# Performance work log

Hardware: AMD Instinct MI355X
Metric: run time of the kernel (lower is better)

Reference implementation:

```python
import jax, jax.numpy as jnp
import numpy as np

VOCAB, E, H, P, B, S = 30522, 1024, 1024, 16, 32, 256
HD = H // 2  # per-direction LSTM hidden


def _lstm_dir(xt, Wih, Whh, bih, bhh, reverse):
    # xt: [S,B,in]; PyTorch gate order i,f,g,o
    Hd = Whh.shape[1]
    Bz = xt.shape[1]
    bias = bih + bhh

    def step(carry, xb):
        h, c = carry
        g = xb @ Wih.T + h @ Whh.T + bias
        i, f, gg, o = jnp.split(g, 4, axis=-1)
        c = jax.nn.sigmoid(f) * c + jax.nn.sigmoid(i) * jnp.tanh(gg)
        h = jax.nn.sigmoid(o) * jnp.tanh(c)
        return (h, c), h

    init = (jnp.zeros((Bz, Hd), xt.dtype), jnp.zeros((Bz, Hd), xt.dtype))
    _, hs = jax.lax.scan(step, init, xt, reverse=reverse)
    return hs  # [S,B,Hd], time-ordered


def _bilstm(x, Wih, Whh, bih, bhh):
    # x: [B,S,in]; Wih: [2,4*HD,in] (dir 0 = fwd, dir 1 = bwd)
    xt = jnp.swapaxes(x, 0, 1)
    fw = _lstm_dir(xt, Wih[0], Whh[0], bih[0], bhh[0], False)
    bw = _lstm_dir(xt, Wih[1], Whh[1], bih[1], bhh[1], True)
    return jnp.swapaxes(jnp.concatenate([fw, bw], axis=-1), 0, 1)  # [B,S,2*HD]


def setup_inputs() -> dict:
    key = jax.random.key(0)
    ks = jax.random.split(key, 20)
    sc = 0.05
    inp = {}
    inp["emb"] = jax.random.normal(ks[0], (VOCAB, E), jnp.float32) * sc
    inp["ctx_emb"] = jax.random.normal(ks[1], (VOCAB, E), jnp.float32) * sc
    inp["prompt_emb"] = jax.random.normal(ks[2], (P, E), jnp.float32) * sc
    # LSTM layer 0: input E; layer 1: input 2*HD = H
    inp["Wih0"] = jax.random.normal(ks[3], (2, 4 * HD, E), jnp.float32) * sc
    inp["Whh0"] = jax.random.normal(ks[4], (2, 4 * HD, HD), jnp.float32) * sc
    inp["bih0"] = jax.random.normal(ks[5], (2, 4 * HD), jnp.float32) * sc
    inp["bhh0"] = jax.random.normal(ks[6], (2, 4 * HD), jnp.float32) * sc
    inp["Wih1"] = jax.random.normal(ks[7], (2, 4 * HD, H), jnp.float32) * sc
    inp["Whh1"] = jax.random.normal(ks[8], (2, 4 * HD, HD), jnp.float32) * sc
    inp["bih1"] = jax.random.normal(ks[9], (2, 4 * HD), jnp.float32) * sc
    inp["bhh1"] = jax.random.normal(ks[10], (2, 4 * HD), jnp.float32) * sc
    inp["W1"] = jax.random.normal(ks[11], (H, H), jnp.float32) * sc
    inp["b1"] = jnp.zeros((H,), jnp.float32)
    inp["W2"] = jax.random.normal(ks[12], (E, H), jnp.float32) * sc
    inp["b2"] = jnp.zeros((E,), jnp.float32)
    inp["input_ids"] = jax.random.randint(ks[13], (B, S), 0, VOCAB)
    # distinct, sorted prompt positions per batch row (torch loop assumes valid slots)
    pk = jax.random.split(ks[14], B)
    perms = jax.vmap(lambda k: jax.random.permutation(k, S)[:P])(pk)
    inp["prompt_indexes"] = jnp.sort(perms, axis=1)
    return inp


def reference(emb, ctx_emb, prompt_emb, Wih0, Whh0, bih0, bhh0,
              Wih1, Whh1, bih1, bhh1, W1, b1, W2, b2,
              input_ids, prompt_indexes):
    raw = emb[input_ids]                               # [B,S,E]
    b_idx = jnp.arange(input_ids.shape[0])[:, None]    # [B,1]
    # unique_prompt branch: detached raw + ctx embedding, scatter prompt embeds
    allb = jax.lax.stop_gradient(raw) + ctx_emb[input_ids]
    allb = allb.at[b_idx, prompt_indexes].set(
        jnp.broadcast_to(prompt_emb, (input_ids.shape[0],) + prompt_emb.shape))
    h = _bilstm(allb, Wih0, Whh0, bih0, bhh0)
    h = _bilstm(h, Wih1, Whh1, bih1, bhh1)             # [B,S,H]
    out = jax.nn.relu(h @ W1.T + b1) @ W2.T + b2       # [B,S,E]
    upd = out[b_idx, prompt_indexes] + prompt_emb      # [B,P,E]
    return raw.at[b_idx, prompt_indexes].set(upd)
```

## Files before the change

### kernel.cpp

```cpp
#include <hip/hip_runtime.h>
#include <hip/hip_bf16.h>
#include <math.h>

constexpr int NB  = 32;
constexpr int NS  = 256;
constexpr int NE  = 1024;
constexpr int NH  = 1024;
constexpr int NHD = 512;
constexpr int NG  = 2048;
constexpr int NP  = 16;
constexpr int NBS = NB * NS;
constexpr int GK  = 1024;

constexpr int UPW  = 16;
constexpr int NWGD = NHD / UPW;
constexpr size_t GT_DIR = (size_t)NWGD * 256 * 2048;

typedef __attribute__((ext_vector_type(8))) short bf16x8;
typedef __attribute__((ext_vector_type(4))) float f32x4;
typedef unsigned short u16;

__device__ __forceinline__ float sigm(float x) { return 1.0f / (1.0f + __expf(-x)); }
__device__ __forceinline__ u16 f2bf(float f) {
    union { float f; unsigned u; } v; v.f = f;
    unsigned r = v.u + 0x7FFF + ((v.u >> 16) & 1);
    return (u16)(r >> 16);
}
__device__ __forceinline__ float bf2f(u16 b) {
    return __uint_as_float((unsigned)b << 16);
}

__global__ void k_zero(int* p) { p[blockIdx.x * 256 + threadIdx.x] = 0; }

__global__ void k_allb(const float* __restrict__ emb, const float* __restrict__ ctx,
                       const float* __restrict__ pemb, const int* __restrict__ ids,
                       const int* __restrict__ pidx, u16* __restrict__ allb) {
    int r = blockIdx.x;
    int b = r >> 8, s = r & 255;
    __shared__ int ppos;
    if (threadIdx.x == 0) {
        int t = -1;
        #pragma unroll
        for (int p = 0; p < NP; ++p)
            if (pidx[b * NP + p] == s) t = p;
        ppos = t;
    }
    __syncthreads();
    int e = threadIdx.x;
    float4 v;
    if (ppos >= 0) {
        v = ((const float4*)(pemb + (size_t)ppos * NE))[e];
    } else {
        int id = ids[r];
        float4 a = ((const float4*)(emb + (size_t)id * NE))[e];
        float4 c = ((const float4*)(ctx + (size_t)id * NE))[e];
        v = make_float4(a.x + c.x, a.y + c.y, a.z + c.z, a.w + c.w);
    }
    ushort4 o;
    o.x = f2bf(v.x); o.y = f2bf(v.y); o.z = f2bf(v.z); o.w = f2bf(v.w);
    *(ushort4*)(allb + ((size_t)(s * NB + b)) * NE + e * 4) = o;
}

__global__ void k_raw(const float* __restrict__ emb, const int* __restrict__ ids,
                      float* __restrict__ out) {
    int r = blockIdx.x;
    int id = ids[r];
    ((float4*)(out + (size_t)r * NE))[threadIdx.x] =
        ((const float4*)(emb + (size_t)id * NE))[threadIdx.x];
}

__global__ void k_wcvt(const float* __restrict__ Wih, const float* __restrict__ bih,
                       const float* __restrict__ bhh, u16* __restrict__ Wbf,
                       float* __restrict__ biasC) {
    int blk = blockIdx.x;
    int d = blk >> 11, np = blk & 2047;
    int rw = (np & 3) * 512 + (np >> 2);
    const float* src = Wih + ((size_t)d * NG + rw) * GK;
    u16* dst = Wbf + ((size_t)d * NG + np) * GK;
    int t = threadIdx.x;
    float4 v = ((const float4*)src)[t];
    ushort4 o;
    o.x = f2bf(v.x); o.y = f2bf(v.y); o.z = f2bf(v.z); o.w = f2bf(v.w);
    ((ushort4*)dst)[t] = o;
    if (t == 0)
        biasC[d * NG + np] = bih[d * NG + rw] + bhh[d * NG + rw];
}

__global__ __launch_bounds__(256) void k_gemm_m(const u16* __restrict__ A0,
                                                const u16* __restrict__ A1,
                                                int astride,
                                                const u16* __restrict__ W,
                                                const float* __restrict__ bc,
                                                float* __restrict__ Gt) {
    __shared__ char At[128 * 128];
    __shared__ char Wt[128 * 128];
    int tid = threadIdx.x;
    int lane = tid & 63, w = tid >> 6;
    int n0 = blockIdx.x * 128, m0 = blockIdx.y * 128;
    int r = tid >> 1, h = tid & 1;

    f32x4 acc[4][4];
    #pragma unroll
    for (int i = 0; i < 4; ++i)
        #pragma unroll
        for (int j = 0; j < 4; ++j) acc[i][j] = (f32x4){0.f, 0.f, 0.f, 0.f};

    unsigned rsw = (unsigned)((r & 7) << 4);
    for (int kt = 0; kt < GK; kt += 64) {
        {
            int k0 = kt + h * 32;
            const u16* asrc = (k0 < 512) ? (A0 + (size_t)(m0 + r) * astride + k0)
                                         : (A1 + (size_t)(m0 + r) * astride + (k0 - 512));
            const u16* wsrc = W + (size_t)(n0 + r) * GK + k0;
            #pragma unroll
            for (int j = 0; j < 4; ++j) {
                uint4 va = *(const uint4*)(asrc + j * 8);
                *(uint4*)(At + r * 128 + (((unsigned)(h * 64 + j * 16)) ^ rsw)) = va;
                uint4 vw = *(const uint4*)(wsrc + j * 8);
                *(uint4*)(Wt + r * 128 + (((unsigned)(h * 64 + j * 16)) ^ rsw)) = vw;
            }
        }
        __syncthreads();
        #pragma unroll
        for (int sub = 0; sub < 2; ++sub) {
            bf16x8 af[4], bfr[4];
            int kbyte = sub * 64 + (lane >> 4) * 16;
            #pragma unroll
            for (int ni = 0; ni < 4; ++ni) {
                int rr = (w & 1) * 64 + ni * 16 + (lane & 15);
                af[ni] = *(const bf16x8*)(Wt + rr * 128 + ((unsigned)kbyte ^ ((unsigned)((rr & 7) << 4))));
            }
            #pragma unroll
            for (int mi = 0; mi < 4; ++mi) {
                int rr = (w >> 1) * 64 + mi * 16 + (lane & 15);
                bfr[mi] = *(const bf16x8*)(At + rr * 128 + ((unsigned)kbyte ^ ((unsigned)((rr & 7) << 4))));
            }
            #pragma unroll
            for (int mi = 0; mi < 4; ++mi)
                #pragma unroll
                for (int ni = 0; ni < 4; ++ni)
                    acc[mi][ni] = __builtin_amdgcn_mfma_f32_16x16x32_bf16(
                        af[ni], bfr[mi], acc[mi][ni], 0, 0, 0);
        }
        __syncthreads();
    }
    #pragma unroll
    for (int mi = 0; mi < 4; ++mi) {
        int mp = m0 + (w >> 1) * 64 + mi * 16 + (lane & 15);
        int t = mp >> 5, b = mp & 31;
        #pragma unroll
        for (int ni = 0; ni < 4; ++ni) {
            int npb = n0 + (w & 1) * 64 + ni * 16 + (lane >> 4) * 4;
            int unit = npb >> 2;
            float4 bv = *(const float4*)(bc + npb);
            f32x4 a = acc[mi][ni];
            float4 o = make_float4(a[0] + bv.x, a[1] + bv.y, a[2] + bv.z, a[3] + bv.w);
            *(float4*)(Gt + ((size_t)((unit >> 4) * NS + t)) * 2048 + b * 64 + (unit & 15) * 4) = o;
        }
    }
}

__global__ __launch_bounds__(256) void k_lstm_p(const float* __restrict__ Gt,
                                                const float* __restrict__ Whh,
                                                u16* __restrict__ hxb,
                                                int* __restrict__ cblk) {
    __shared__ char hlds[NB * NHD * 2];
    int wg = blockIdx.x;
    int d = wg & 1;
    int slice = wg >> 1;
    int n0 = slice * UPW;
    int tid = threadIdx.x;
    int lane = tid & 63;
    int w = tid >> 6;
    int* lines  = cblk + d * 512;
    int* myline = lines + slice * 16;
    int pollidx = (lane & 31) * 16;
    u16* hxd = hxb + (size_t)d * NS * NB * NHD;
    const float* Gd = Gt + (size_t)d * GT_DIR + (size_t)slice * NS * 2048;

    bf16x8 wfrag[16];
    {
        int rloc = lane & 15;
        int usub = rloc >> 2, g = rloc & 3;
        int kb = lane >> 4;
        const float* wrow = Whh + ((size_t)d * NG + g * NHD + n0 + 4 * w + usub) * NHD;
        #pragma unroll
        for (int kk = 0; kk < 16; ++kk) {
            const float* p = wrow + kk * 32 + kb * 8;
            float4 x = *(const float4*)p;
            float4 y = *(const float4*)(p + 4);
            bf16x8 wf;
            wf[0] = (short)f2bf(x.x); wf[1] = (short)f2bf(x.y);
            wf[2] = (short)f2bf(x.z); wf[3] = (short)f2bf(x.w);
            wf[4] = (short)f2bf(y.x); wf[5] = (short)f2bf(y.y);
            wf[6] = (short)f2bf(y.z); wf[7] = (short)f2bf(y.w);
            wfrag[kk] = wf;
        }
    }
    int uloc  = 4 * w + (lane >> 4);
    int unitC = n0 + uloc;
    int bcol0 = lane & 15;
    int bcol1 = 16 + bcol0;
    int kb    = lane >> 4;
    int c8 = tid & 7, bRow = tid >> 3;

    float c0 = 0.f, c1 = 0.f;
    int ttp = d ? (NS - 1) : 0;
    float4 Gv0 = *(const float4*)(Gd + (size_t)ttp * 2048 + bcol0 * 64 + uloc * 4);
    float4 Gv1 = *(const float4*)(Gd + (size_t)ttp * 2048 + bcol1 * 64 + uloc * 4);

    for (int step = 0; step < NS; ++step) {
        int tt = d ? (NS - 1 - step) : step;
        f32x4 acc0 = {0.f, 0.f, 0.f, 0.f};
        f32x4 acc1 = {0.f, 0.f, 0.f, 0.f};
        if (step) {
            int tprev = d ? tt + 1 : tt - 1;
            const u16* srow = hxd + ((size_t)tprev * NB + bRow) * NHD;
            char* dstrow = hlds + bRow * 1024;
            unsigned rsw = (unsigned)((bRow & 7) << 4);
            #pragma unroll
            for (int i = 0; i < 8; ++i) {
                uint4 v = *(const uint4*)(srow + c8 * 64 + i * 8);
                *(uint4*)(dstrow + (((unsigned)(c8 * 128 + i * 16)) ^ rsw)) = v;
            }
            __syncthreads();
            const char* b0base = hlds + bcol0 * 1024;
            const char* b1base = hlds + bcol1 * 1024;
            unsigned s0 = (unsigned)((bcol0 & 7) << 4);
            unsigned s1 = (unsigned)((bcol1 & 7) << 4);
            #pragma unroll
            for (int kk = 0; kk < 16; ++kk) {
                bf16x8 b0 = *(const bf16x8*)(b0base + (((unsigned)(kk * 64 + kb * 16)) ^ s0));
                bf16x8 b1 = *(const bf16x8*)(b1base + (((unsigned)(kk * 64 + kb * 16)) ^ s1));
                acc0 = __builtin_amdgcn_mfma_f32_16x16x32_bf16(wfrag[kk], b0, acc0, 0, 0, 0);
                acc1 = __builtin_amdgcn_mfma_f32_16x16x32_bf16(wfrag[kk], b1, acc1, 0, 0, 0);
            }
        }
        {
            float ig = sigm(acc0[0] + Gv0.x);
            float fg = sigm(acc0[1] + Gv0.y);
            float gg = tanhf(acc0[2] + Gv0.z);
            float og = sigm(acc0[3] + Gv0.w);
            c0 = fg * c0 + ig * gg;
            float hv = og * tanhf(c0);
            __hip_atomic_store(hxd + ((size_t)tt * NB + bcol0) * NHD + unitC, f2bf(hv),
                               __ATOMIC_RELAXED, __HIP_MEMORY_SCOPE_AGENT);
        }
        {
            float ig = sigm(acc1[0] + Gv1.x);
            float fg = sigm(acc1[1] + Gv1.y);
            float gg = tanhf(acc1[2] + Gv1.z);
            float og = sigm(acc1[3] + Gv1.w);
            c1 = fg * c1 + ig * gg;
            float hv = og * tanhf(c1);
            __hip_atomic_store(hxd + ((size_t)tt * NB + bcol1) * NHD + unitC, f2bf(hv),
                               __ATOMIC_RELAXED, __HIP_MEMORY_SCOPE_AGENT);
        }
        if (step == NS - 1) break;
        asm volatile("s_waitcnt vmcnt(0)" ::: "memory");
        __syncthreads();
        if (tid == 0)
            __hip_atomic_store(myline, step + 1, __ATOMIC_RELAXED,
                               __HIP_MEMORY_SCOPE_AGENT);
        {
            int ttn = d ? tt - 1 : tt + 1;
            Gv0 = *(const float4*)(Gd + (size_t)ttn * 2048 + bcol0 * 64 + uloc * 4);
            Gv1 = *(const float4*)(Gd + (size_t)ttn * 2048 + bcol1 * 64 + uloc * 4);
        }
        asm volatile("" ::: "memory");
        {
            int target = step + 1;
            for (;;) {
                int v = __hip_atomic_load(lines + pollidx, __ATOMIC_RELAXED,
                                          __HIP_MEMORY_SCOPE_AGENT);
                if (__all(v >= target)) break;
                __builtin_amdgcn_s_sleep(1);
            }
        }
    }
}

__global__ __launch_bounds__(256) void k_mlp1(const u16* __restrict__ hxb,
                                              const int* __restrict__ pidx,
                                              const float* __restrict__ W1,
                                              const float* __restrict__ b1,
                                              float* __restrict__ mid) {
    __shared__ float As[16][65];
    __shared__ float Ws[16][65];
    int tid = threadIdx.x;
    int tx = tid & 15, ty = tid >> 4;
    int n0 = blockIdx.x * 64, m0 = blockIdx.y * 64;
    int lr = tid >> 2;
    int lk = (tid & 3) * 4;
    int m = m0 + lr;
    int bb = m >> 4;
    int s = pidx[m];
    float acc[4][4] = {};
    for (int kt = 0; kt < GK; kt += 16) {
        int k0 = kt + lk;
        int half = k0 >> 9;
        ushort4 av4 = *(const ushort4*)(hxb + (((size_t)(half * NS + s)) * NB + bb) * NHD + (k0 & 511));
        float4 wv = *(const float4*)(W1 + (size_t)(n0 + lr) * GK + k0);
        As[lk + 0][lr] = bf2f(av4.x); As[lk + 1][lr] = bf2f(av4.y);
        As[lk + 2][lr] = bf2f(av4.z); As[lk + 3][lr] = bf2f(av4.w);
        Ws[lk + 0][lr] = wv.x; Ws[lk + 1][lr] = wv.y;
        Ws[lk + 2][lr] = wv.z; Ws[lk + 3][lr] = wv.w;
        __syncthreads();
        #pragma unroll
        for (int kk = 0; kk < 16; ++kk) {
            float a[4], wv2[4];
            #pragma unroll
            for (int i = 0; i < 4; ++i) a[i] = As[kk][ty * 4 + i];
            #pragma unroll
            for (int j = 0; j < 4; ++j) wv2[j] = Ws[kk][tx * 4 + j];
            #pragma unroll
            for (int i = 0; i < 4; ++i)
                #pragma unroll
                for (int j = 0; j < 4; ++j) acc[i][j] += a[i] * wv2[j];
        }
        __syncthreads();
    }
    #pragma unroll
    for (int j = 0; j < 4; ++j) {
        int n = n0 + tx * 4 + j;
        float bias = b1[n];
        #pragma unroll
        for (int i = 0; i < 4; ++i)
            mid[(size_t)(m0 + ty * 4 + i) * 1024 + n] = fmaxf(acc[i][j] + bias, 0.f);
    }
}

__global__ __launch_bounds__(256) void k_mlp2(const float* __restrict__ mid,
                                              const int* __restrict__ pidx,
                                              const float* __restrict__ W2,
                                              const float* __restrict__ b2,
                                              const float* __restrict__ pemb,
                                              float* __restrict__ out) {
    __shared__ float As[16][65];
    __shared__ float Ws[16][65];
    int tid = threadIdx.x;
    int tx = tid & 15, ty = tid >> 4;
    int n0 = blockIdx.x * 64, m0 = blockIdx.y * 64;
    int lr = tid >> 2;
    int lk = (tid & 3) * 4;
    float acc[4][4] = {};
    for (int kt = 0; kt < GK; kt += 16) {
        float4 av = *(const float4*)(mid + (size_t)(m0 + lr) * GK + kt + lk);
        float4 wv = *(const float4*)(W2 + (size_t)(n0 + lr) * GK + kt + lk);
        As[lk + 0][lr] = av.x; As[lk + 1][lr] = av.y;
        As[lk + 2][lr] = av.z; As[lk + 3][lr] = av.w;
        Ws[lk + 0][lr] = wv.x; Ws[lk + 1][lr] = wv.y;
        Ws[lk + 2][lr] = wv.z; Ws[lk + 3][lr] = wv.w;
        __syncthreads();
        #pragma unroll
        for (int kk = 0; kk < 16; ++kk) {
            float a[4], wv2[4];
            #pragma unroll
            for (int i = 0; i < 4; ++i) a[i] = As[kk][ty * 4 + i];
            #pragma unroll
            for (int j = 0; j < 4; ++j) wv2[j] = Ws[kk][tx * 4 + j];
            #pragma unroll
            for (int i = 0; i < 4; ++i)
                #pragma unroll
                for (int j = 0; j < 4; ++j) acc[i][j] += a[i] * wv2[j];
        }
        __syncthreads();
    }
    #pragma unroll
    for (int i = 0; i < 4; ++i) {
        int m = m0 + ty * 4 + i;
        int bb = m >> 4, p = m & 15;
        int s = pidx[m];
        float* orow = out + ((size_t)(bb * NS + s)) * NE;
        const float* prow = pemb + (size_t)p * NE;
        #pragma unroll
        for (int j = 0; j < 4; ++j) {
            int n = n0 + tx * 4 + j;
            orow[n] = acc[i][j] + b2[n] + prow[n];
        }
    }
}

extern "C" void kernel_launch(void* const* d_in, const int* in_sizes, int n_in,
                              void* d_out, int out_size, void* d_ws, size_t ws_size,
                              hipStream_t stream) {
    const float* emb  = (const float*)d_in[0];
    const float* ctx  = (const float*)d_in[1];
    const float* pemb = (const float*)d_in[2];
    const float* Wih0 = (const float*)d_in[3];
    const float* Whh0 = (const float*)d_in[4];
    const float* bih0 = (const float*)d_in[5];
    const float* bhh0 = (const float*)d_in[6];
    const float* Wih1 = (const float*)d_in[7];
    const float* Whh1 = (const float*)d_in[8];
    const float* bih1 = (const float*)d_in[9];
    const float* bhh1 = (const float*)d_in[10];
    const float* W1   = (const float*)d_in[11];
    const float* b1   = (const float*)d_in[12];
    const float* W2   = (const float*)d_in[13];
    const float* b2   = (const float*)d_in[14];
    const int* ids    = (const int*)d_in[15];
    const int* pidx   = (const int*)d_in[16];
    float* out = (float*)d_out;

    char* ws = (char*)d_ws;
    float* Gt    = (float*)ws;
    u16*   allb  = (u16*)(ws + 134217728u);
    u16*   hx    = (u16*)(ws + 150994944u);
    u16*   Wbf   = (u16*)(ws + 167772160u);
    float* biasC = (float*)(ws + 176160768u);
    float* mid   = (float*)(ws + 176177152u);
    int*   ctr   = (int*)(ws + 178274304u);

    k_zero<<<dim3(8), dim3(256), 0, stream>>>(ctr);
    k_allb<<<dim3(NBS), dim3(256), 0, stream>>>(emb, ctx, pemb, ids, pidx, allb);

    k_wcvt<<<dim3(2 * NG), dim3(256), 0, stream>>>(Wih0, bih0, bhh0, Wbf, biasC);
    for (int d = 0; d < 2; ++d)
        k_gemm_m<<<dim3(NG / 128, NBS / 128), dim3(256), 0, stream>>>(
            allb, allb + 512, 1024, Wbf + (size_t)d * NG * GK, biasC + d * NG,
            Gt + (size_t)d * GT_DIR);
    k_lstm_p<<<dim3(2 * NWGD), dim3(256), 0, stream>>>(Gt, Whh0, hx, ctr);

    k_raw<<<dim3(NBS), dim3(256), 0, stream>>>(emb, ids, out);

    k_wcvt<<<dim3(2 * NG), dim3(256), 0, stream>>>(Wih1, bih1, bhh1, Wbf, biasC);
    for (int d = 0; d < 2; ++d)
        k_gemm_m<<<dim3(NG / 128, NBS / 128), dim3(256), 0, stream>>>(
            hx, hx + (size_t)NS * NB * NHD, 512, Wbf + (size_t)d * NG * GK,
            biasC + d * NG, Gt + (size_t)d * GT_DIR);
    k_lstm_p<<<dim3(2 * NWGD), dim3(256), 0, stream>>>(Gt, Whh1, hx, ctr + 1024);

    k_mlp1<<<dim3(16, 8), dim3(256), 0, stream>>>(hx, pidx, W1, b1, mid);
    k_mlp2<<<dim3(16, 8), dim3(256), 0, stream>>>(mid, pidx, W2, b2, pemb, out);
}
```

Baseline: 2.363 ms.

## Double LSTM units per workgroup to halve recurrent WG count, use fast tanh

The persistent LSTM recurrence kernel now handles 32 hidden units per workgroup with 512 threads, so each direction uses 16 workgroups instead of 32. The gate-buffer layout in the GEMM epilogue changes to match, and each workgroup still stages the full h tile into LDS. This cuts the number of workgroups that must poll the cross-workgroup barrier each timestep, which reduces sync latency. tanh and sigmoid switch to fast exp/fdividef forms, trading some accuracy for cheaper transcendentals in the serial critical path.

```diff
diff --git a/kernel.cpp b/kernel.cpp
--- a/kernel.cpp
+++ b/kernel.cpp
@@ -12,15 +12,22 @@
 constexpr int NBS = NB * NS;
 constexpr int GK  = 1024;
 
-constexpr int UPW  = 16;
+constexpr int UPW  = 32;
 constexpr int NWGD = NHD / UPW;
-constexpr size_t GT_DIR = (size_t)NWGD * 256 * 2048;
+constexpr size_t GT_DIR = (size_t)NWGD * 256 * 4096;
 
 typedef __attribute__((ext_vector_type(8))) short bf16x8;
 typedef __attribute__((ext_vector_type(4))) float f32x4;
 typedef unsigned short u16;
-
-__device__ __forceinline__ float sigm(float x) { return 1.0f / (1.0f + __expf(-x)); }
+typedef unsigned long long u64;
+
+__device__ __forceinline__ float sigm(float x) {
+    return __fdividef(1.0f, 1.0f + __expf(-x));
+}
+__device__ __forceinline__ float tanhfast(float x) {
+    float t = __expf(2.0f * x);
+    return 1.0f - __fdividef(2.0f, t + 1.0f);
+}
 __device__ __forceinline__ u16 f2bf(float f) {
     union { float f; unsigned u; } v; v.f = f;
     unsigned r = v.u + 0x7FFF + ((v.u >> 16) & 1);
@@ -155,12 +162,12 @@
             float4 bv = *(const float4*)(bc + npb);
             f32x4 a = acc[mi][ni];
             float4 o = make_float4(a[0] + bv.x, a[1] + bv.y, a[2] + bv.z, a[3] + bv.w);
-            *(float4*)(Gt + ((size_t)((unit >> 4) * NS + t)) * 2048 + b * 64 + (unit & 15) * 4) = o;
-        }
-    }
-}
-
-__global__ __launch_bounds__(256) void k_lstm_p(const float* __restrict__ Gt,
+            *(float4*)(Gt + ((size_t)((unit >> 5) * NS + t)) * 4096 + b * 128 + (unit & 31) * 4) = o;
+        }
+    }
+}
+
+__global__ __launch_bounds__(512) void k_lstm_v(const float* __restrict__ Gt,
                                                 const float* __restrict__ Whh,
                                                 u16* __restrict__ hxb,
                                                 int* __restrict__ cblk) {
@@ -172,21 +179,21 @@
     int tid = threadIdx.x;
     int lane = tid & 63;
     int w = tid >> 6;
-    int* lines  = cblk + d * 512;
+    int* lines  = cblk + d * 256;
     int* myline = lines + slice * 16;
-    int pollidx = (lane & 31) * 16;
+    int pollidx = (lane & 15) * 16;
     u16* hxd = hxb + (size_t)d * NS * NB * NHD;
-    const float* Gd = Gt + (size_t)d * GT_DIR + (size_t)slice * NS * 2048;
+    const float* Gd = Gt + (size_t)d * GT_DIR + (size_t)slice * NS * 4096;
 
     bf16x8 wfrag[16];
     {
         int rloc = lane & 15;
         int usub = rloc >> 2, g = rloc & 3;
-        int kb = lane >> 4;
+        int kb0 = lane >> 4;
         const float* wrow = Whh + ((size_t)d * NG + g * NHD + n0 + 4 * w + usub) * NHD;
         #pragma unroll
         for (int kk = 0; kk < 16; ++kk) {
-            const float* p = wrow + kk * 32 + kb * 8;
+            const float* p = wrow + kk * 32 + kb0 * 8;
             float4 x = *(const float4*)p;
             float4 y = *(const float4*)(p + 4);
             bf16x8 wf;
@@ -202,12 +209,15 @@
     int bcol0 = lane & 15;
     int bcol1 = 16 + bcol0;
     int kb    = lane >> 4;
-    int c8 = tid & 7, bRow = tid >> 3;
+    int sRow = tid >> 4, c4 = tid & 15;
+    unsigned rsw = (unsigned)((sRow & 7) << 4);
+    unsigned s0 = (unsigned)((bcol0 & 7) << 4);
+    unsigned s1 = (unsigned)((bcol1 & 7) << 4);
 
     float c0 = 0.f, c1 = 0.f;
     int ttp = d ? (NS - 1) : 0;
-    float4 Gv0 = *(const float4*)(Gd + (size_t)ttp * 2048 + bcol0 * 64 + uloc * 4);
-    float4 Gv1 = *(const float4*)(Gd + (size_t)ttp * 2048 + bcol1 * 64 + uloc * 4);
+    float4 Gv0 = *(const float4*)(Gd + (size_t)ttp * 4096 + bcol0 * 128 + uloc * 4);
+    float4 Gv1 = *(const float4*)(Gd + (size_t)ttp * 4096 + bcol1 * 128 + uloc * 4);
 
     for (int step = 0; step < NS; ++step) {
         int tt = d ? (NS - 1 - step) : step;
@@ -215,19 +225,16 @@
         f32x4 acc1 = {0.f, 0.f, 0.f, 0.f};
         if (step) {
             int tprev = d ? tt + 1 : tt - 1;
-            const u16* srow = hxd + ((size_t)tprev * NB + bRow) * NHD;
-            char* dstrow = hlds + bRow * 1024;
-            unsigned rsw = (unsigned)((bRow & 7) << 4);
-            #pragma unroll
-            for (int i = 0; i < 8; ++i) {
-                uint4 v = *(const uint4*)(srow + c8 * 64 + i * 8);
-                *(uint4*)(dstrow + (((unsigned)(c8 * 128 + i * 16)) ^ rsw)) = v;
+            const u16* srow = hxd + ((size_t)tprev * NB + sRow) * NHD + c4 * 32;
+            char* dstrow = hlds + sRow * 1024;
+            #pragma unroll
+            for (int i = 0; i < 4; ++i) {
+                uint4 v = *(const uint4*)(srow + i * 8);
+                *(uint4*)(dstrow + (((unsigned)(c4 * 64 + i * 16)) ^ rsw)) = v;
             }
             __syncthreads();
             const char* b0base = hlds + bcol0 * 1024;
             const char* b1base = hlds + bcol1 * 1024;
-            unsigned s0 = (unsigned)((bcol0 & 7) << 4);
-            unsigned s1 = (unsigned)((bcol1 & 7) << 4);
             #pragma unroll
             for (int kk = 0; kk < 16; ++kk) {
                 bf16x8 b0 = *(const bf16x8*)(b0base + (((unsigned)(kk * 64 + kb * 16)) ^ s0));
@@ -239,20 +246,20 @@
         {
             float ig = sigm(acc0[0] + Gv0.x);
             float fg = sigm(acc0[1] + Gv0.y);
-            float gg = tanhf(acc0[2] + Gv0.z);
+            float gg = tanhfast(acc0[2] + Gv0.z);
             float og = sigm(acc0[3] + Gv0.w);
             c0 = fg * c0 + ig * gg;
-            float hv = og * tanhf(c0);
+            float hv = og * tanhfast(c0);
             __hip_atomic_store(hxd + ((size_t)tt * NB + bcol0) * NHD + unitC, f2bf(hv),
                                __ATOMIC_RELAXED, __HIP_MEMORY_SCOPE_AGENT);
         }
         {
             float ig = sigm(acc1[0] + Gv1.x);
             float fg = sigm(acc1[1] + Gv1.y);
-            float gg = tanhf(acc1[2] + Gv1.z);
+            float gg = tanhfast(acc1[2] + Gv1.z);
             float og = sigm(acc1[3] + Gv1.w);
             c1 = fg * c1 + ig * gg;
-            float hv = og * tanhf(c1);
+            float hv = og * tanhfast(c1);
             __hip_atomic_store(hxd + ((size_t)tt * NB + bcol1) * NHD + unitC, f2bf(hv),
                                __ATOMIC_RELAXED, __HIP_MEMORY_SCOPE_AGENT);
         }
@@ -264,8 +271,8 @@
                                __HIP_MEMORY_SCOPE_AGENT);
         {
             int ttn = d ? tt - 1 : tt + 1;
-            Gv0 = *(const float4*)(Gd + (size_t)ttn * 2048 + bcol0 * 64 + uloc * 4);
-            Gv1 = *(const float4*)(Gd + (size_t)ttn * 2048 + bcol1 * 64 + uloc * 4);
+            Gv0 = *(const float4*)(Gd + (size_t)ttn * 4096 + bcol0 * 128 + uloc * 4);
+            Gv1 = *(const float4*)(Gd + (size_t)ttn * 4096 + bcol1 * 128 + uloc * 4);
         }
         asm volatile("" ::: "memory");
         {
@@ -412,7 +419,7 @@
     float* mid   = (float*)(ws + 176177152u);
     int*   ctr   = (int*)(ws + 178274304u);
 
-    k_zero<<<dim3(8), dim3(256), 0, stream>>>(ctr);
+    k_zero<<<dim3(4), dim3(256), 0, stream>>>(ctr);
     k_allb<<<dim3(NBS), dim3(256), 0, stream>>>(emb, ctx, pemb, ids, pidx, allb);
 
     k_wcvt<<<dim3(2 * NG), dim3(256), 0, stream>>>(Wih0, bih0, bhh0, Wbf, biasC);
@@ -420,7 +427,7 @@
         k_gemm_m<<<dim3(NG / 128, NBS / 128), dim3(256), 0, stream>>>(
             allb, allb + 512, 1024, Wbf + (size_t)d * NG * GK, biasC + d * NG,
             Gt + (size_t)d * GT_DIR);
-    k_lstm_p<<<dim3(2 * NWGD), dim3(256), 0, stream>>>(Gt, Whh0, hx, ctr);
+    k_lstm_v<<<dim3(2 * NWGD), dim3(512), 0, stream>>>(Gt, Whh0, hx, ctr);
 
     k_raw<<<dim3(NBS), dim3(256), 0, stream>>>(emb, ids, out);
 
@@ -429,7 +436,7 @@
         k_gemm_m<<<dim3(NG / 128, NBS / 128), dim3(256), 0, stream>>>(
             hx, hx + (size_t)NS * NB * NHD, 512, Wbf + (size_t)d * NG * GK,
             biasC + d * NG, Gt + (size_t)d * GT_DIR);
-    k_lstm_p<<<dim3(2 * NWGD), dim3(256), 0, stream>>>(Gt, Whh1, hx, ctr + 1024);
+    k_lstm_v<<<dim3(2 * NWGD), dim3(512), 0, stream>>>(Gt, Whh1, hx, ctr + 512);
 
     k_mlp1<<<dim3(16, 8), dim3(256), 0, stream>>>(hx, pidx, W1, b1, mid);
     k_mlp2<<<dim3(16, 8), dim3(256), 0, stream>>>(mid, pidx, W2, b2, pemb, out);
```

New measurement: 2.409 ms. No clear change (+2.0%).

## Fuse input-projection GEMM with LSTM recurrence via per-timestep-group readiness counters

Applied to the files above, without the earlier changes.

Merges the input-gate GEMM and the persistent LSTM recurrence into one launch. GEMM blocks publish completion counters per 128-row (4-timestep) group, ordered so each direction's needed timesteps are produced first, and the recurrence blocks spin on those counters before reading gate preactivations. This lets the serial recurrence start while the GEMM is still running. The raw-embedding copy is folded into the same launch, and the layer-1 output gets its own buffer (reusing allb). Sigmoid and tanh switch to fast exp/divide approximations. The design depends on the 64 recurrence workgroups being resident and scheduled ahead of the GEMM blocks; otherwise it can deadlock or lose the overlap.

```diff
diff --git a/kernel.cpp b/kernel.cpp
--- a/kernel.cpp
+++ b/kernel.cpp
@@ -19,8 +19,15 @@
 typedef __attribute__((ext_vector_type(8))) short bf16x8;
 typedef __attribute__((ext_vector_type(4))) float f32x4;
 typedef unsigned short u16;
-
-__device__ __forceinline__ float sigm(float x) { return 1.0f / (1.0f + __expf(-x)); }
+typedef unsigned long long u64;
+
+__device__ __forceinline__ float sigm(float x) {
+    return __fdividef(1.0f, 1.0f + __expf(-x));
+}
+__device__ __forceinline__ float tanhfast(float x) {
+    float t = __expf(2.0f * x);
+    return 1.0f - __fdividef(2.0f, t + 1.0f);
+}
 __device__ __forceinline__ u16 f2bf(float f) {
     union { float f; unsigned u; } v; v.f = f;
     unsigned r = v.u + 0x7FFF + ((v.u >> 16) & 1);
@@ -59,14 +66,6 @@
     ushort4 o;
     o.x = f2bf(v.x); o.y = f2bf(v.y); o.z = f2bf(v.z); o.w = f2bf(v.w);
     *(ushort4*)(allb + ((size_t)(s * NB + b)) * NE + e * 4) = o;
-}
-
-__global__ void k_raw(const float* __restrict__ emb, const int* __restrict__ ids,
-                      float* __restrict__ out) {
-    int r = blockIdx.x;
-    int id = ids[r];
-    ((float4*)(out + (size_t)r * NE))[threadIdx.x] =
-        ((const float4*)(emb + (size_t)id * NE))[threadIdx.x];
 }
 
 __global__ void k_wcvt(const float* __restrict__ Wih, const float* __restrict__ bih,
@@ -86,94 +85,120 @@
         biasC[d * NG + np] = bih[d * NG + rw] + bhh[d * NG + rw];
 }
 
-__global__ __launch_bounds__(256) void k_gemm_m(const u16* __restrict__ A0,
-                                                const u16* __restrict__ A1,
-                                                int astride,
-                                                const u16* __restrict__ W,
-                                                const float* __restrict__ bc,
-                                                float* __restrict__ Gt) {
-    __shared__ char At[128 * 128];
-    __shared__ char Wt[128 * 128];
+__global__ __launch_bounds__(256) void k_mega(
+        const u16* __restrict__ A0, const u16* __restrict__ A1, int astride,
+        const u16* __restrict__ Wbf, const float* __restrict__ biasC,
+        float* __restrict__ Gt, const float* __restrict__ Whh,
+        u16* __restrict__ hxb, int* __restrict__ ctrL,
+        const float* __restrict__ emb, const int* __restrict__ ids,
+        float* __restrict__ rawout) {
+    __shared__ char smem[32768];
+    int wg = blockIdx.x;
     int tid = threadIdx.x;
-    int lane = tid & 63, w = tid >> 6;
-    int n0 = blockIdx.x * 128, m0 = blockIdx.y * 128;
-    int r = tid >> 1, h = tid & 1;
-
-    f32x4 acc[4][4];
-    #pragma unroll
-    for (int i = 0; i < 4; ++i)
-        #pragma unroll
-        for (int j = 0; j < 4; ++j) acc[i][j] = (f32x4){0.f, 0.f, 0.f, 0.f};
-
-    unsigned rsw = (unsigned)((r & 7) << 4);
-    for (int kt = 0; kt < GK; kt += 64) {
-        {
-            int k0 = kt + h * 32;
-            const u16* asrc = (k0 < 512) ? (A0 + (size_t)(m0 + r) * astride + k0)
-                                         : (A1 + (size_t)(m0 + r) * astride + (k0 - 512));
-            const u16* wsrc = W + (size_t)(n0 + r) * GK + k0;
-            #pragma unroll
-            for (int j = 0; j < 4; ++j) {
-                uint4 va = *(const uint4*)(asrc + j * 8);
-                *(uint4*)(At + r * 128 + (((unsigned)(h * 64 + j * 16)) ^ rsw)) = va;
-                uint4 vw = *(const uint4*)(wsrc + j * 8);
-                *(uint4*)(Wt + r * 128 + (((unsigned)(h * 64 + j * 16)) ^ rsw)) = vw;
-            }
-        }
-        __syncthreads();
-        #pragma unroll
-        for (int sub = 0; sub < 2; ++sub) {
-            bf16x8 af[4], bfr[4];
-            int kbyte = sub * 64 + (lane >> 4) * 16;
+
+    if (wg >= 2112) {
+        int r = wg - 2112;
+        int id = ids[r];
+        ((float4*)(rawout + (size_t)r * NE))[tid] =
+            ((const float4*)(emb + (size_t)id * NE))[tid];
+        return;
+    }
+
+    if (wg >= 64) {
+        char* At = smem;
+        char* Wt = smem + 16384;
+        int gb  = wg - 64;
+        int ord = gb >> 5;
+        int rem = gb & 31;
+        int d   = rem & 1;
+        int bx  = rem >> 1;
+        int by  = d ? (63 - ord) : ord;
+        const u16* W = Wbf + (size_t)d * NG * GK;
+        const float* bc = biasC + d * NG;
+        float* Gd = Gt + (size_t)d * GT_DIR;
+        int lane = tid & 63, w = tid >> 6;
+        int n0 = bx * 128, m0 = by * 128;
+        int r = tid >> 1, h = tid & 1;
+
+        f32x4 acc[4][4];
+        #pragma unroll
+        for (int i = 0; i < 4; ++i)
+            #pragma unroll
+            for (int j = 0; j < 4; ++j) acc[i][j] = (f32x4){0.f, 0.f, 0.f, 0.f};
+
+        unsigned rsw = (unsigned)((r & 7) << 4);
+        for (int kt = 0; kt < GK; kt += 64) {
+            {
+                int k0 = kt + h * 32;
+                const u16* asrc = (k0 < 512) ? (A0 + (size_t)(m0 + r) * astride + k0)
+                                             : (A1 + (size_t)(m0 + r) * astride + (k0 - 512));
+                const u16* wsrc = W + (size_t)(n0 + r) * GK + k0;
+                #pragma unroll
+                for (int j = 0; j < 4; ++j) {
+                    uint4 va = *(const uint4*)(asrc + j * 8);
+                    *(uint4*)(At + r * 128 + (((unsigned)(h * 64 + j * 16)) ^ rsw)) = va;
+                    uint4 vw = *(const uint4*)(wsrc + j * 8);
+                    *(uint4*)(Wt + r * 128 + (((unsigned)(h * 64 + j * 16)) ^ rsw)) = vw;
+                }
+            }
+            __syncthreads();
+            #pragma unroll
+            for (int sub = 0; sub < 2; ++sub) {
+                bf16x8 af[4], bfr[4];
+                int kbyte = sub * 64 + (lane >> 4) * 16;
+                #pragma unroll
+                for (int ni = 0; ni < 4; ++ni) {
+                    int rr = (w & 1) * 64 + ni * 16 + (lane & 15);
+                    af[ni] = *(const bf16x8*)(Wt + rr * 128 + ((unsigned)kbyte ^ ((unsigned)((rr & 7) << 4))));
+                }
+                #pragma unroll
+                for (int mi = 0; mi < 4; ++mi) {
+                    int rr = (w >> 1) * 64 + mi * 16 + (lane & 15);
+                    bfr[mi] = *(const bf16x8*)(At + rr * 128 + ((unsigned)kbyte ^ ((unsigned)((rr & 7) << 4))));
+                }
+                #pragma unroll
+                for (int mi = 0; mi < 4; ++mi)
+                    #pragma unroll
+                    for (int ni = 0; ni < 4; ++ni)
+                        acc[mi][ni] = __builtin_amdgcn_mfma_f32_16x16x32_bf16(
+                            af[ni], bfr[mi], acc[mi][ni], 0, 0, 0);
+            }
+            __syncthreads();
+        }
+        #pragma unroll
+        for (int mi = 0; mi < 4; ++mi) {
+            int mp = m0 + (w >> 1) * 64 + mi * 16 + (lane & 15);
+            int t = mp >> 5, b = mp & 31;
             #pragma unroll
             for (int ni = 0; ni < 4; ++ni) {
-                int rr = (w & 1) * 64 + ni * 16 + (lane & 15);
-                af[ni] = *(const bf16x8*)(Wt + rr * 128 + ((unsigned)kbyte ^ ((unsigned)((rr & 7) << 4))));
-            }
-            #pragma unroll
-            for (int mi = 0; mi < 4; ++mi) {
-                int rr = (w >> 1) * 64 + mi * 16 + (lane & 15);
-                bfr[mi] = *(const bf16x8*)(At + rr * 128 + ((unsigned)kbyte ^ ((unsigned)((rr & 7) << 4))));
-            }
-            #pragma unroll
-            for (int mi = 0; mi < 4; ++mi)
-                #pragma unroll
-                for (int ni = 0; ni < 4; ++ni)
-                    acc[mi][ni] = __builtin_amdgcn_mfma_f32_16x16x32_bf16(
-                        af[ni], bfr[mi], acc[mi][ni], 0, 0, 0);
-        }
-        __syncthreads();
-    }
-    #pragma unroll
-    for (int mi = 0; mi < 4; ++mi) {
-        int mp = m0 + (w >> 1) * 64 + mi * 16 + (lane & 15);
-        int t = mp >> 5, b = mp & 31;
-        #pragma unroll
-        for (int ni = 0; ni < 4; ++ni) {
-            int npb = n0 + (w & 1) * 64 + ni * 16 + (lane >> 4) * 4;
-            int unit = npb >> 2;
-            float4 bv = *(const float4*)(bc + npb);
-            f32x4 a = acc[mi][ni];
-            float4 o = make_float4(a[0] + bv.x, a[1] + bv.y, a[2] + bv.z, a[3] + bv.w);
-            *(float4*)(Gt + ((size_t)((unit >> 4) * NS + t)) * 2048 + b * 64 + (unit & 15) * 4) = o;
-        }
-    }
-}
-
-__global__ __launch_bounds__(256) void k_lstm_p(const float* __restrict__ Gt,
-                                                const float* __restrict__ Whh,
-                                                u16* __restrict__ hxb,
-                                                int* __restrict__ cblk) {
-    __shared__ char hlds[NB * NHD * 2];
-    int wg = blockIdx.x;
+                int npb = n0 + (w & 1) * 64 + ni * 16 + (lane >> 4) * 4;
+                int unit = npb >> 2;
+                float4 bv = *(const float4*)(bc + npb);
+                f32x4 a = acc[mi][ni];
+                union { float4 f; u64 q[2]; } cv;
+                cv.f = make_float4(a[0] + bv.x, a[1] + bv.y, a[2] + bv.z, a[3] + bv.w);
+                float* p = Gd + ((size_t)((unit >> 4) * NS + t)) * 2048 + b * 64 + (unit & 15) * 4;
+                __hip_atomic_store((u64*)p,     cv.q[0], __ATOMIC_RELAXED, __HIP_MEMORY_SCOPE_AGENT);
+                __hip_atomic_store((u64*)p + 1, cv.q[1], __ATOMIC_RELAXED, __HIP_MEMORY_SCOPE_AGENT);
+            }
+        }
+        asm volatile("s_waitcnt vmcnt(0)" ::: "memory");
+        __syncthreads();
+        if (tid == 0)
+            __hip_atomic_fetch_add(ctrL + 1024 + (d * 64 + by) * 16, 1,
+                                   __ATOMIC_RELAXED, __HIP_MEMORY_SCOPE_AGENT);
+        return;
+    }
+
+    char* hlds = smem;
     int d = wg & 1;
     int slice = wg >> 1;
     int n0 = slice * UPW;
-    int tid = threadIdx.x;
     int lane = tid & 63;
     int w = tid >> 6;
-    int* lines  = cblk + d * 512;
+    int* lines  = ctrL + d * 512;
     int* myline = lines + slice * 16;
+    int* gcnt   = ctrL + 1024;
     int pollidx = (lane & 31) * 16;
     u16* hxd = hxb + (size_t)d * NS * NB * NHD;
     const float* Gd = Gt + (size_t)d * GT_DIR + (size_t)slice * NS * 2048;
@@ -182,11 +207,11 @@
     {
         int rloc = lane & 15;
         int usub = rloc >> 2, g = rloc & 3;
-        int kb = lane >> 4;
+        int kb0 = lane >> 4;
         const float* wrow = Whh + ((size_t)d * NG + g * NHD + n0 + 4 * w + usub) * NHD;
         #pragma unroll
         for (int kk = 0; kk < 16; ++kk) {
-            const float* p = wrow + kk * 32 + kb * 8;
+            const float* p = wrow + kk * 32 + kb0 * 8;
             float4 x = *(const float4*)p;
             float4 y = *(const float4*)(p + 4);
             bf16x8 wf;
@@ -203,9 +228,20 @@
     int bcol1 = 16 + bcol0;
     int kb    = lane >> 4;
     int c8 = tid & 7, bRow = tid >> 3;
+    unsigned rsw = (unsigned)((bRow & 7) << 4);
+    unsigned s0 = (unsigned)((bcol0 & 7) << 4);
+    unsigned s1 = (unsigned)((bcol1 & 7) << 4);
 
     float c0 = 0.f, c1 = 0.f;
+    int gReady = -1;
     int ttp = d ? (NS - 1) : 0;
+    {
+        int g0 = ttp >> 2;
+        int* gl = gcnt + (d * 64 + g0) * 16;
+        while (__hip_atomic_load(gl, __ATOMIC_RELAXED, __HIP_MEMORY_SCOPE_AGENT) < 16)
+            __builtin_amdgcn_s_sleep(1);
+        gReady = g0;
+    }
     float4 Gv0 = *(const float4*)(Gd + (size_t)ttp * 2048 + bcol0 * 64 + uloc * 4);
     float4 Gv1 = *(const float4*)(Gd + (size_t)ttp * 2048 + bcol1 * 64 + uloc * 4);
 
@@ -217,7 +253,6 @@
             int tprev = d ? tt + 1 : tt - 1;
             const u16* srow = hxd + ((size_t)tprev * NB + bRow) * NHD;
             char* dstrow = hlds + bRow * 1024;
-            unsigned rsw = (unsigned)((bRow & 7) << 4);
             #pragma unroll
             for (int i = 0; i < 8; ++i) {
                 uint4 v = *(const uint4*)(srow + c8 * 64 + i * 8);
@@ -226,8 +261,6 @@
             __syncthreads();
             const char* b0base = hlds + bcol0 * 1024;
             const char* b1base = hlds + bcol1 * 1024;
-            unsigned s0 = (unsigned)((bcol0 & 7) << 4);
-            unsigned s1 = (unsigned)((bcol1 & 7) << 4);
             #pragma unroll
             for (int kk = 0; kk < 16; ++kk) {
                 bf16x8 b0 = *(const bf16x8*)(b0base + (((unsigned)(kk * 64 + kb * 16)) ^ s0));
@@ -239,20 +272,20 @@
         {
             float ig = sigm(acc0[0] + Gv0.x);
             float fg = sigm(acc0[1] + Gv0.y);
-            float gg = tanhf(acc0[2] + Gv0.z);
+            float gg = tanhfast(acc0[2] + Gv0.z);
             float og = sigm(acc0[3] + Gv0.w);
             c0 = fg * c0 + ig * gg;
-            float hv = og * tanhf(c0);
+            float hv = og * tanhfast(c0);
             __hip_atomic_store(hxd + ((size_t)tt * NB + bcol0) * NHD + unitC, f2bf(hv),
                                __ATOMIC_RELAXED, __HIP_MEMORY_SCOPE_AGENT);
         }
         {
             float ig = sigm(acc1[0] + Gv1.x);
             float fg = sigm(acc1[1] + Gv1.y);
-            float gg = tanhf(acc1[2] + Gv1.z);
+            float gg = tanhfast(acc1[2] + Gv1.z);
             float og = sigm(acc1[3] + Gv1.w);
             c1 = fg * c1 + ig * gg;
-            float hv = og * tanhf(c1);
+            float hv = og * tanhfast(c1);
             __hip_atomic_store(hxd + ((size_t)tt * NB + bcol1) * NHD + unitC, f2bf(hv),
                                __ATOMIC_RELAXED, __HIP_MEMORY_SCOPE_AGENT);
         }
@@ -264,6 +297,13 @@
                                __HIP_MEMORY_SCOPE_AGENT);
         {
             int ttn = d ? tt - 1 : tt + 1;
+            int g = ttn >> 2;
+            if (g != gReady) {
+                int* gl = gcnt + (d * 64 + g) * 16;
+                while (__hip_atomic_load(gl, __ATOMIC_RELAXED, __HIP_MEMORY_SCOPE_AGENT) < 16)
+                    __builtin_amdgcn_s_sleep(1);
+                gReady = g;
+            }
             Gv0 = *(const float4*)(Gd + (size_t)ttn * 2048 + bcol0 * 64 + uloc * 4);
             Gv1 = *(const float4*)(Gd + (size_t)ttn * 2048 + bcol1 * 64 + uloc * 4);
         }
@@ -406,31 +446,26 @@
     char* ws = (char*)d_ws;
     float* Gt    = (float*)ws;
     u16*   allb  = (u16*)(ws + 134217728u);
-    u16*   hx    = (u16*)(ws + 150994944u);
+    u16*   hx0   = (u16*)(ws + 150994944u);
     u16*   Wbf   = (u16*)(ws + 167772160u);
     float* biasC = (float*)(ws + 176160768u);
     float* mid   = (float*)(ws + 176177152u);
     int*   ctr   = (int*)(ws + 178274304u);
-
-    k_zero<<<dim3(8), dim3(256), 0, stream>>>(ctr);
+    u16*   hx1   = allb;
+
+    k_zero<<<dim3(24), dim3(256), 0, stream>>>(ctr);
     k_allb<<<dim3(NBS), dim3(256), 0, stream>>>(emb, ctx, pemb, ids, pidx, allb);
 
     k_wcvt<<<dim3(2 * NG), dim3(256), 0, stream>>>(Wih0, bih0, bhh0, Wbf, biasC);
-    for (int d = 0; d < 2; ++d)
-        k_gemm_m<<<dim3(NG / 128, NBS / 128), dim3(256), 0, stream>>>(
-            allb, allb + 512, 1024, Wbf + (size_t)d * NG * GK, biasC + d * NG,
-            Gt + (size_t)d * GT_DIR);
-    k_lstm_p<<<dim3(2 * NWGD), dim3(256), 0, stream>>>(Gt, Whh0, hx, ctr);
-
-    k_raw<<<dim3(NBS), dim3(256), 0, stream>>>(emb, ids, out);
+    k_mega<<<dim3(64 + 2048 + NBS), dim3(256), 0, stream>>>(
+        allb, allb + 512, 1024, Wbf, biasC, Gt, Whh0, hx0, ctr,
+        emb, ids, out);
 
     k_wcvt<<<dim3(2 * NG), dim3(256), 0, stream>>>(Wih1, bih1, bhh1, Wbf, biasC);
-    for (int d = 0; d < 2; ++d)
-        k_gemm_m<<<dim3(NG / 128, NBS / 128), dim3(256), 0, stream>>>(
-            hx, hx + (size_t)NS * NB * NHD, 512, Wbf + (size_t)d * NG * GK,
-            biasC + d * NG, Gt + (size_t)d * GT_DIR);
-    k_lstm_p<<<dim3(2 * NWGD), dim3(256), 0, stream>>>(Gt, Whh1, hx, ctr + 1024);
-
-    k_mlp1<<<dim3(16, 8), dim3(256), 0, stream>>>(hx, pidx, W1, b1, mid);
+    k_mega<<<dim3(64 + 2048), dim3(256), 0, stream>>>(
+        hx0, hx0 + (size_t)NS * NB * NHD, 512, Wbf, biasC, Gt, Whh1, hx1,
+        ctr + 3072, emb, ids, out);
+
+    k_mlp1<<<dim3(16, 8), dim3(256), 0, stream>>>(hx1, pidx, W1, b1, mid);
     k_mlp2<<<dim3(16, 8), dim3(256), 0, stream>>>(mid, pidx, W2, b2, pemb, out);
 }
```

New measurement: 2.200 ms. -6.9%, faster.
